# Performance work log

Hardware: AMD Instinct MI355X
Metric: run time of the kernel (lower is better)

## Reference

```python
import jax, jax.numpy as jnp
import numpy as np

N = 100000
E = 1600000
H = 128
L = 3


def setup_inputs() -> dict:
    key = jax.random.key(0)
    ks = jax.random.split(key, 8)
    z = jax.random.normal(ks[0], (N, H), dtype=jnp.float32)
    edge_index = jax.random.randint(ks[1], (2, E), 0, N, dtype=jnp.int64)
    edge_weight = jax.random.uniform(ks[2], (E,), dtype=jnp.float32)
    s = 1.0 / np.sqrt(H)
    weight = jax.random.uniform(ks[3], (L, H, H), minval=-s, maxval=s, dtype=jnp.float32)
    w_ih = jax.random.uniform(ks[4], (3 * H, H), minval=-s, maxval=s, dtype=jnp.float32)
    w_hh = jax.random.uniform(ks[5], (3 * H, H), minval=-s, maxval=s, dtype=jnp.float32)
    b_ih = jax.random.uniform(ks[6], (3 * H,), minval=-s, maxval=s, dtype=jnp.float32)
    b_hh = jax.random.uniform(ks[7], (3 * H,), minval=-s, maxval=s, dtype=jnp.float32)
    return {"z": z, "edge_weight": edge_weight, "weight": weight,
            "w_ih": w_ih, "w_hh": w_hh, "b_ih": b_ih, "b_hh": b_hh,
            "edge_index": edge_index}


def _gru_cell(m, h, w_ih, w_hh, b_ih, b_hh):
    # torch GRUCell: gate order (r, z, n)
    gi = m @ w_ih.T + b_ih   # [N, 3H]
    gh = h @ w_hh.T + b_hh   # [N, 3H]
    i_r, i_z, i_n = jnp.split(gi, 3, axis=-1)
    h_r, h_z, h_n = jnp.split(gh, 3, axis=-1)
    r = jax.nn.sigmoid(i_r + h_r)
    zg = jax.nn.sigmoid(i_z + h_z)
    n = jnp.tanh(i_n + r * h_n)
    return (1.0 - zg) * n + zg * h


def reference(z, edge_weight, weight, w_ih, w_hh, b_ih, b_hh, edge_index):
    src = edge_index[0]  # x_j gathered from source nodes
    dst = edge_index[1]  # aggregated at target nodes
    x = z  # in_channels == out_channels, so no zero padding needed
    for l in range(L):
        m = x @ weight[l]                                  # [N, H]
        msg = m[src] * edge_weight[:, None]                # [E, H]
        agg = jax.ops.segment_sum(msg, dst, num_segments=N)  # aggr='add'
        x = _gru_cell(agg, x, w_ih, w_hh, b_ih, b_hh)
    return x
```

## Files before the change

kernel.cpp:

```cpp
#include <hip/hip_runtime.h>

typedef __bf16 bf16x8 __attribute__((ext_vector_type(8)));
typedef float floatx4 __attribute__((ext_vector_type(4)));

#define NPB 256
#define NPB_SHIFT 8
#define MAXNB 1024
#define TILE 2048

static __device__ __forceinline__ float bfu_to_f(unsigned short u) {
    unsigned int x = ((unsigned int)u) << 16;
    return __builtin_bit_cast(float, x);
}
static __device__ __forceinline__ unsigned short f_to_bfu(float f) {
    unsigned int u = __builtin_bit_cast(unsigned int, f);
    unsigned int r = (u + 0x7fffu + ((u >> 16) & 1u)) >> 16;
    return (unsigned short)r;
}

__global__ void detect_k(const unsigned short* __restrict__ bih_u,
                         const unsigned int* __restrict__ ei_u,
                         int* __restrict__ flags) {
    __shared__ int sv, sz;
    int t = threadIdx.x;
    if (t == 0) { sv = 0; sz = 0; }
    __syncthreads();
    unsigned short u = bih_u[2 * t];
    unsigned int ex = (u >> 7) & 0xFF;
    if (ex >= 64 && ex < 124) atomicAdd(&sv, 1);
    if (ei_u[2 * t + 1] == 0u) atomicAdd(&sz, 1);
    __syncthreads();
    if (t == 0) {
        flags[0] = (sv >= 48) ? 1 : 0;
        flags[1] = (sz == 64) ? 1 : 0;
    }
}


__global__ void cvt_bf16_k(const void* __restrict__ in, unsigned short* __restrict__ out,
                           int n, const int* __restrict__ flags) {
    int i = blockIdx.x * 256 + threadIdx.x;
    if (i >= n) return;
    if (flags[0]) out[i] = ((const unsigned short*)in)[i];
    else out[i] = f_to_bfu(((const float*)in)[i]);
}

__global__ void cvt_bias_k(const void* __restrict__ bih, const void* __restrict__ bhh,
                           float* __restrict__ bih_f, float* __restrict__ bhh_f,
                           const int* __restrict__ flags) {
    int i = blockIdx.x * 256 + threadIdx.x;
    if (i >= 768) return;
    const void* src = (i < 384) ? bih : bhh;
    int j = (i < 384) ? i : i - 384;
    float v = flags[0] ? bfu_to_f(((const unsigned short*)src)[j]) : ((const float*)src)[j];
    if (i < 384) bih_f[j] = v;
    else bhh_f[j] = v;
}

__global__ void out_k(const unsigned short* __restrict__ xb, void* __restrict__ out,
                      int n, const int* __restrict__ flags) {
    int i = blockIdx.x * 256 + threadIdx.x;
    if (i >= n) return;
    if (flags[0]) ((unsigned short*)out)[i] = xb[i];
    else ((float*)out)[i] = bfu_to_f(xb[i]);
}


static __device__ __forceinline__ int load_idx(const unsigned int* eiu, size_t pos, int is64) {
    return (int)eiu[is64 ? 2 * pos : pos];
}

__global__ __launch_bounds__(256) void count_k(const unsigned int* __restrict__ eiu,
                                               int* __restrict__ bucketCnt, int E,
                                               const int* __restrict__ flags) {
    __shared__ int cnt[MAXNB];
    int t = threadIdx.x;
    for (int b = t; b < MAXNB; b += 256) cnt[b] = 0;
    __syncthreads();
    int is64 = flags[1];
    int e0 = blockIdx.x * TILE;
    int e1 = min(e0 + TILE, E);
    for (int e = e0 + t; e < e1; e += 256) {
        int d = load_idx(eiu, (size_t)E + e, is64);
        atomicAdd(&cnt[d >> NPB_SHIFT], 1);
    }
    __syncthreads();
    for (int b = t; b < MAXNB; b += 256) {
        int c = cnt[b];
        if (c) atomicAdd(&bucketCnt[b], c);
    }
}

__global__ void scanB_k(const int* __restrict__ bucketCnt, int* __restrict__ bucketBase,
                        int* __restrict__ bucketCursor, int NB, int E) {
    __shared__ int sh[MAXNB];
    int t = threadIdx.x;
    int v = (t < NB) ? bucketCnt[t] : 0;
    sh[t] = v;
    __syncthreads();
    for (int off = 1; off < MAXNB; off <<= 1) {
        int u = (t >= off) ? sh[t - off] : 0;
        __syncthreads();
        sh[t] += u;
        __syncthreads();
    }
    if (t < NB) {
        int b = sh[t] - v;
        bucketBase[t] = b;
        bucketCursor[t] = b;
    }
    if (t == 0) bucketBase[NB] = E;
}

__global__ __launch_bounds__(256) void bin_k(const unsigned int* __restrict__ eiu,
                                             const void* __restrict__ ew,
                                             int* __restrict__ bucketCursor,
                                             uint2* __restrict__ rec8,
                                             int* __restrict__ dstA, int E,
                                             const int* __restrict__ flags) {
    __shared__ int cnt[MAXNB];
    __shared__ int basel[MAXNB];
    int t = threadIdx.x;
    for (int b = t; b < MAXNB; b += 256) cnt[b] = 0;
    __syncthreads();
    int is64 = flags[1];
    int isb = flags[0];
    int e0 = blockIdx.x * TILE;
    int e1 = min(e0 + TILE, E);
    for (int e = e0 + t; e < e1; e += 256) {
        int d = load_idx(eiu, (size_t)E + e, is64);
        atomicAdd(&cnt[d >> NPB_SHIFT], 1);
    }
    __syncthreads();
    for (int b = t; b < MAXNB; b += 256) {
        int c = cnt[b];
        basel[b] = c ? atomicAdd(&bucketCursor[b], c) : 0;
        cnt[b] = 0;
    }
    __syncthreads();
    for (int e = e0 + t; e < e1; e += 256) {
        int s = load_idx(eiu, (size_t)e, is64);
        int d = load_idx(eiu, (size_t)E + e, is64);
        float w = isb ? bfu_to_f(((const unsigned short*)ew)[e]) : ((const float*)ew)[e];
        int b = d >> NPB_SHIFT;
        int p = basel[b] + atomicAdd(&cnt[b], 1);
        dstA[p] = d;
        rec8[p] = make_uint2((unsigned int)s, __builtin_bit_cast(unsigned int, w));
    }
}

__global__ __launch_bounds__(256) void csr_k(const uint2* __restrict__ rec8,
                                             const int* __restrict__ dstA,
                                             const int* __restrict__ bucketBase,
                                             int* __restrict__ offsets,
                                             uint2* __restrict__ rec, int N, int E) {
    __shared__ int cnt[NPB];
    __shared__ int sh[NPB];
    __shared__ int cur[NPB];
    int t = threadIdx.x;
    int b = blockIdx.x;
    int n0 = b << NPB_SHIFT;
    int nodes = min(NPB, N - n0);
    int ebase = bucketBase[b];
    int ecnt = bucketBase[b + 1] - ebase;

    cnt[t] = 0;
    __syncthreads();
    for (int i = t; i < ecnt; i += 256) {
        int d = dstA[ebase + i] - n0;
        atomicAdd(&cnt[d], 1);
    }
    __syncthreads();
    int v = cnt[t];
    sh[t] = v;
    __syncthreads();
    for (int off = 1; off < NPB; off <<= 1) {
        int u = (t >= off) ? sh[t - off] : 0;
        __syncthreads();
        sh[t] += u;
        __syncthreads();
    }
    int loff = sh[t] - v;
    if (t < nodes) offsets[n0 + t] = ebase + loff;
    cur[t] = ebase + loff;
    if (b == 0 && t == 0) offsets[N] = E;
    __syncthreads();
    for (int i = t; i < ecnt; i += 256) {
        int d = dstA[ebase + i] - n0;
        int p = atomicAdd(&cur[d], 1);
        rec[p] = rec8[ebase + i];
    }
}


static __device__ __forceinline__ float dot8_bf(uint4 wv, uint4 iv) {
    float s;
    s  = bfu_to_f((unsigned short)(wv.x)) * bfu_to_f((unsigned short)(iv.x));
    s += bfu_to_f((unsigned short)(wv.x >> 16)) * bfu_to_f((unsigned short)(iv.x >> 16));
    s += bfu_to_f((unsigned short)(wv.y)) * bfu_to_f((unsigned short)(iv.y));
    s += bfu_to_f((unsigned short)(wv.y >> 16)) * bfu_to_f((unsigned short)(iv.y >> 16));
    s += bfu_to_f((unsigned short)(wv.z)) * bfu_to_f((unsigned short)(iv.z));
    s += bfu_to_f((unsigned short)(wv.z >> 16)) * bfu_to_f((unsigned short)(iv.z >> 16));
    s += bfu_to_f((unsigned short)(wv.w)) * bfu_to_f((unsigned short)(iv.w));
    s += bfu_to_f((unsigned short)(wv.w >> 16)) * bfu_to_f((unsigned short)(iv.w >> 16));
    return s;
}

__global__ void make_ut_k(const void* __restrict__ weight, const void* __restrict__ wih,
                          unsigned short* __restrict__ Ut, const int* __restrict__ flags) {
    int idx = blockIdx.x * 256 + threadIdx.x;
    if (idx >= 3 * 384 * 128) return;
    int isb = flags[0];
    int a = idx & 127;
    int j = (idx >> 7) % 384;
    int l = idx / (384 * 128);
    float s = 0.f;
    if (isb) {
        const uint4* W4 = (const uint4*)((const unsigned short*)weight + (size_t)l * 16384 + a * 128);
        const uint4* I4 = (const uint4*)((const unsigned short*)wih + (size_t)j * 128);
#pragma unroll
        for (int c = 0; c < 16; c++) s += dot8_bf(W4[c], I4[c]);
    } else {
        const float4* W4 = (const float4*)((const float*)weight + (size_t)l * 16384 + a * 128);
        const float4* I4 = (const float4*)((const float*)wih + (size_t)j * 128);
#pragma unroll
        for (int c = 0; c < 32; c++) {
            float4 w = W4[c], i = I4[c];
            s += w.x * i.x + w.y * i.y + w.z * i.z + w.w * i.w;
        }
    }
    Ut[idx] = f_to_bfu(s);
}

__global__ void pack_b_k(const unsigned short* __restrict__ Ut,
                         const void* __restrict__ whh,
                         unsigned short* __restrict__ Bp,
                         const int* __restrict__ flags) {
    int idx = blockIdx.x * 256 + threadIdx.x;
    if (idx >= 3 * 4 * 12 * 4 * 64) return;
    int lane = idx & 63;
    int kc = (idx >> 6) & 3;
    int rest = idx >> 8;
    int j = rest % 12;
    int cg = (rest / 12) & 3;
    int l = rest / 48;
    int s = j / 6;
    int g = (j % 6) >> 1;
    int t = j & 1;
    int col = (cg * 2 + t) * 16 + (lane & 15);
    int k = kc * 32 + (lane >> 4) * 8;
    int row384 = g * 128 + col;
    unsigned short tmp[8];
    const unsigned short* src;
    if (s == 0) {
        src = Ut + (size_t)l * 49152 + row384 * 128 + k;
    } else if (flags[0]) {
        src = (const unsigned short*)whh + (size_t)row384 * 128 + k;
    } else {
        const float* wf = (const float*)whh + (size_t)row384 * 128 + k;
        for (int i = 0; i < 8; i++) tmp[i] = f_to_bfu(wf[i]);
        src = tmp;
    }
    unsigned short* dst = Bp + (size_t)l * 98304 + (((size_t)(cg * 12 + j) * 4 + kc) * 64 + lane) * 8;
    for (int i = 0; i < 8; i++) dst[i] = src[i];
}


__global__ __launch_bounds__(256) void agg_k(const unsigned short* __restrict__ xb,
                                             const int* __restrict__ offs,
                                             const uint2* __restrict__ rec,
                                             unsigned short* __restrict__ y, int N) {
    int node = (int)((blockIdx.x * 256 + threadIdx.x) >> 4);
    int l16 = threadIdx.x & 15;
    if (node >= N) return;
    int b = offs[node];
    int e2 = offs[node + 1];
    const uint4* xp4 = (const uint4*)xb;
    float a0[8], a1[8];
#pragma unroll
    for (int i = 0; i < 8; i++) { a0[i] = 0.f; a1[i] = 0.f; }

    auto fma_row = [&](float* acc, uint4 v, float w) {
        acc[0] += w * __builtin_bit_cast(float, v.x << 16);
        acc[1] += w * __builtin_bit_cast(float, v.x & 0xffff0000u);
        acc[2] += w * __builtin_bit_cast(float, v.y << 16);
        acc[3] += w * __builtin_bit_cast(float, v.y & 0xffff0000u);
        acc[4] += w * __builtin_bit_cast(float, v.z << 16);
        acc[5] += w * __builtin_bit_cast(float, v.z & 0xffff0000u);
        acc[6] += w * __builtin_bit_cast(float, v.w << 16);
        acc[7] += w * __builtin_bit_cast(float, v.w & 0xffff0000u);
    };

    int e = b;
    for (; e + 4 <= e2; e += 4) {
        uint2 r0 = rec[e], r1 = rec[e + 1], r2 = rec[e + 2], r3 = rec[e + 3];
        uint4 v0 = xp4[(size_t)r0.x * 16 + l16];
        uint4 v1 = xp4[(size_t)r1.x * 16 + l16];
        uint4 v2 = xp4[(size_t)r2.x * 16 + l16];
        uint4 v3 = xp4[(size_t)r3.x * 16 + l16];
        fma_row(a0, v0, __builtin_bit_cast(float, r0.y));
        fma_row(a1, v1, __builtin_bit_cast(float, r1.y));
        fma_row(a0, v2, __builtin_bit_cast(float, r2.y));
        fma_row(a1, v3, __builtin_bit_cast(float, r3.y));
    }
    for (; e < e2; e++) {
        uint2 r = rec[e];
        uint4 v = xp4[(size_t)r.x * 16 + l16];
        fma_row(a0, v, __builtin_bit_cast(float, r.y));
    }

    uint4 o;
    o.x = (unsigned int)f_to_bfu(a0[0] + a1[0]) | ((unsigned int)f_to_bfu(a0[1] + a1[1]) << 16);
    o.y = (unsigned int)f_to_bfu(a0[2] + a1[2]) | ((unsigned int)f_to_bfu(a0[3] + a1[3]) << 16);
    o.z = (unsigned int)f_to_bfu(a0[4] + a1[4]) | ((unsigned int)f_to_bfu(a0[5] + a1[5]) << 16);
    o.w = (unsigned int)f_to_bfu(a0[6] + a1[6]) | ((unsigned int)f_to_bfu(a0[7] + a1[7]) << 16);
    ((uint4*)y)[(size_t)node * 16 + l16] = o;
}


__global__ __launch_bounds__(512, 4) void gru_k(const unsigned short* __restrict__ y,
                                                const unsigned short* __restrict__ xin,
                                                unsigned short* __restrict__ xout,
                                                const unsigned short* __restrict__ Bp,
                                                const float* __restrict__ bih,
                                                const float* __restrict__ bhh, int N) {
    __shared__ uint4 Blds[3072];

    int bid = blockIdx.x;
    int r8 = bid & 7;
    int inner = bid >> 3;
    int cg = inner & 3;
    int rb = ((inner >> 2) << 3) + r8;
    int row0 = rb << 7;
    if (row0 >= N) return;

    int tid = threadIdx.x;
    {
        const uint4* bsrc = (const uint4*)(Bp + (size_t)cg * 24576);
#pragma unroll
        for (int i = 0; i < 6; i++) Blds[tid + i * 512] = bsrc[tid + i * 512];
    }
    __syncthreads();

    int wave = tid >> 6;
    int wc = wave & 1;
    int wr = wave >> 1;
    int lane = tid & 63;
    int quad = lane >> 4;
    int m16 = lane & 15;
    const unsigned short* bl = (const unsigned short*)Blds;

    int rA[2];
#pragma unroll
    for (int rt = 0; rt < 2; rt++) {
        int r = row0 + wr * 32 + rt * 16 + m16;
        rA[rt] = (r < N) ? r : N - 1;
    }

    floatx4 acc[2][4];
#pragma unroll
    for (int rt = 0; rt < 2; rt++)
#pragma unroll
        for (int s = 0; s < 4; s++) acc[rt][s] = (floatx4){0.f, 0.f, 0.f, 0.f};

    bf16x8 aY[2][4], aX[2][4];

#pragma unroll
    for (int rt = 0; rt < 2; rt++)
#pragma unroll
        for (int kc = 0; kc < 4; kc++)
            aY[rt][kc] = *(const bf16x8*)(y + (size_t)rA[rt] * 128 + kc * 32 + quad * 8);
    __builtin_amdgcn_sched_barrier(0);

#pragma unroll
    for (int rt = 0; rt < 2; rt++)
#pragma unroll
        for (int kc = 0; kc < 4; kc++)
            aX[rt][kc] = *(const bf16x8*)(xin + (size_t)rA[rt] * 128 + kc * 32 + quad * 8);

#pragma unroll
    for (int kc = 0; kc < 4; kc++) {
#pragma unroll
        for (int g = 0; g < 3; g++) {
            int jU = g * 2 + wc;
            bf16x8 b = *(const bf16x8*)(bl + ((size_t)(jU * 4 + kc) * 64 + lane) * 8);
            int s = (g == 2) ? 2 : g;
            acc[0][s] = __builtin_amdgcn_mfma_f32_16x16x32_bf16(aY[0][kc], b, acc[0][s], 0, 0, 0);
            acc[1][s] = __builtin_amdgcn_mfma_f32_16x16x32_bf16(aY[1][kc], b, acc[1][s], 0, 0, 0);
        }
    }
    __builtin_amdgcn_sched_barrier(0);

#pragma unroll
    for (int kc = 0; kc < 4; kc++) {
#pragma unroll
        for (int g = 0; g < 3; g++) {
            int jW = 6 + g * 2 + wc;
            bf16x8 b = *(const bf16x8*)(bl + ((size_t)(jW * 4 + kc) * 64 + lane) * 8);
            int s = (g == 2) ? 3 : g;
            acc[0][s] = __builtin_amdgcn_mfma_f32_16x16x32_bf16(aX[0][kc], b, acc[0][s], 0, 0, 0);
            acc[1][s] = __builtin_amdgcn_mfma_f32_16x16x32_bf16(aX[1][kc], b, acc[1][s], 0, 0, 0);
        }
    }

    int ch = cg * 32 + wc * 16 + m16;
    float b_r = bih[ch] + bhh[ch];
    float b_z = bih[128 + ch] + bhh[128 + ch];
    float bi_n = bih[256 + ch];
    float bh_n = bhh[256 + ch];
#pragma unroll
    for (int rt = 0; rt < 2; rt++) {
#pragma unroll
        for (int ri = 0; ri < 4; ri++) {
            int row = row0 + wr * 32 + rt * 16 + quad * 4 + ri;
            if (row >= N) continue;
            float sr = acc[rt][0][ri] + b_r;
            float sz = acc[rt][1][ri] + b_z;
            float gn = acc[rt][2][ri] + bi_n;
            float hn = acc[rt][3][ri] + bh_n;
            float r = __builtin_amdgcn_rcpf(1.f + __expf(-sr));
            float zg = __builtin_amdgcn_rcpf(1.f + __expf(-sz));
            float x2 = gn + r * hn;
            float n = 1.f - 2.f * __builtin_amdgcn_rcpf(1.f + __expf(2.f * x2));
            float h = bfu_to_f(xin[(size_t)row * 128 + ch]);
            float o = n + zg * (h - n);
            xout[(size_t)row * 128 + ch] = f_to_bfu(o);
        }
    }
}


extern "C" void kernel_launch(void* const* d_in, const int* in_sizes, int n_in,
                              void* d_out, int out_size, void* d_ws, size_t ws_size,
                              hipStream_t stream) {
    const int N = in_sizes[0] / 128;
    const int E = in_sizes[1];
    const int NB = (N + NPB - 1) >> NPB_SHIFT;

    const void* z = d_in[0];
    const void* ew = d_in[1];
    const void* weight = d_in[2];
    const void* wih = d_in[3];
    const void* whh = d_in[4];
    const void* bih = d_in[5];
    const void* bhh = d_in[6];
    const unsigned int* eiu = (const unsigned int*)d_in[7];

    unsigned short* y = (unsigned short*)d_out;

    size_t off = 0;
    char* base = (char*)d_ws;
    auto carve = [&](size_t bytes) -> void* {
        void* p = base + off;
        off = (off + bytes + 255) & ~(size_t)255;
        return p;
    };
    unsigned short* xb = (unsigned short*)carve((size_t)N * 128 * 2);
    unsigned short* xb2 = (unsigned short*)carve((size_t)N * 128 * 2);
    uint2* rec8 = (uint2*)carve((size_t)E * 8);
    int* dstA = (int*)carve((size_t)E * 4);
    uint2* rec = (uint2*)carve((size_t)E * 8);
    int* offsets = (int*)carve((size_t)(N + 1) * 4);
    int* bucketCnt = (int*)carve(MAXNB * 4);
    int* bucketBase = (int*)carve((MAXNB + 1) * 4);
    int* bucketCursor = (int*)carve(MAXNB * 4);
    unsigned short* Ut = (unsigned short*)carve((size_t)3 * 384 * 128 * 2);
    unsigned short* Bp = (unsigned short*)carve((size_t)3 * 48 * 4 * 64 * 8 * 2);
    float* bih_f = (float*)carve(384 * 4);
    float* bhh_f = (float*)carve(384 * 4);
    int* flags = (int*)carve(256);

    detect_k<<<1, 64, 0, stream>>>((const unsigned short*)bih, eiu, flags);

    cvt_bf16_k<<<(N * 128 + 255) / 256, 256, 0, stream>>>(z, xb, N * 128, flags);
    cvt_bias_k<<<3, 256, 0, stream>>>(bih, bhh, bih_f, bhh_f, flags);

    hipMemsetAsync(bucketCnt, 0, MAXNB * 4, stream);
    int gbin = (E + TILE - 1) / TILE;
    count_k<<<gbin, 256, 0, stream>>>(eiu, bucketCnt, E, flags);
    scanB_k<<<1, MAXNB, 0, stream>>>(bucketCnt, bucketBase, bucketCursor, NB, E);
    bin_k<<<gbin, 256, 0, stream>>>(eiu, ew, bucketCursor, rec8, dstA, E, flags);
    csr_k<<<NB, NPB, 0, stream>>>(rec8, dstA, bucketBase, offsets, rec, N, E);

    make_ut_k<<<(3 * 384 * 128 + 255) / 256, 256, 0, stream>>>(weight, wih, Ut, flags);
    pack_b_k<<<(3 * 4 * 12 * 4 * 64 + 255) / 256, 256, 0, stream>>>(Ut, whh, Bp, flags);

    const int RB = (N + 127) >> 7;
    const int grid_gru = 8 * ((RB + 7) >> 3) * 4;

    const unsigned short* cur = xb;
    unsigned short* nxt = xb2;
    for (int l = 0; l < 3; l++) {
        agg_k<<<(N + 15) / 16, 256, 0, stream>>>(cur, offsets, rec, y, N);
        gru_k<<<grid_gru, 512, 0, stream>>>(y, cur, nxt, Bp + (size_t)l * 98304,
                                            bih_f, bhh_f, N);
        const unsigned short* tmp = cur;
        cur = nxt;
        nxt = (unsigned short*)tmp;
    }

    out_k<<<(N * 128 + 255) / 256, 256, 0, stream>>>(cur, d_out, N * 128, flags);
}
```

Before: 653.1 us.

## Pack local dst into edge records, drop dstA, remap agg blocks across XCDs

Packs the low 8 bits of each edge's destination into the upper bits of the source index inside the binned edge record, so the separate dstA array is no longer written or read during CSR construction. This cuts preprocessing memory traffic. It also doubles the binning tile size and permutes agg_k block IDs so consecutive node chunks land on the same XCD, aiming for better L2 locality on offsets and edge records. The risks are that source indices must fit in 20 bits (true for N=100000), and padding blocks that exit early add a little launch overhead.

```diff
diff --git a/kernel.cpp b/kernel.cpp
--- a/kernel.cpp
+++ b/kernel.cpp
@@ -6,7 +6,7 @@
 #define NPB 256
 #define NPB_SHIFT 8
 #define MAXNB 1024
-#define TILE 2048
+#define TILE 4096
 
 static __device__ __forceinline__ float bfu_to_f(unsigned short u) {
     unsigned int x = ((unsigned int)u) << 16;
@@ -115,8 +115,7 @@
 __global__ __launch_bounds__(256) void bin_k(const unsigned int* __restrict__ eiu,
                                              const void* __restrict__ ew,
                                              int* __restrict__ bucketCursor,
-                                             uint2* __restrict__ rec8,
-                                             int* __restrict__ dstA, int E,
+                                             uint2* __restrict__ rec8, int E,
                                              const int* __restrict__ flags) {
     __shared__ int cnt[MAXNB];
     __shared__ int basel[MAXNB];
@@ -144,13 +143,12 @@
         float w = isb ? bfu_to_f(((const unsigned short*)ew)[e]) : ((const float*)ew)[e];
         int b = d >> NPB_SHIFT;
         int p = basel[b] + atomicAdd(&cnt[b], 1);
-        dstA[p] = d;
-        rec8[p] = make_uint2((unsigned int)s, __builtin_bit_cast(unsigned int, w));
+        rec8[p] = make_uint2((unsigned int)s | ((unsigned int)(d & 255) << 20),
+                             __builtin_bit_cast(unsigned int, w));
     }
 }
 
 __global__ __launch_bounds__(256) void csr_k(const uint2* __restrict__ rec8,
-                                             const int* __restrict__ dstA,
                                              const int* __restrict__ bucketBase,
                                              int* __restrict__ offsets,
                                              uint2* __restrict__ rec, int N, int E) {
@@ -167,7 +165,7 @@
     cnt[t] = 0;
     __syncthreads();
     for (int i = t; i < ecnt; i += 256) {
-        int d = dstA[ebase + i] - n0;
+        int d = (rec8[ebase + i].x >> 20) & 255;
         atomicAdd(&cnt[d], 1);
     }
     __syncthreads();
@@ -186,9 +184,10 @@
     if (b == 0 && t == 0) offsets[N] = E;
     __syncthreads();
     for (int i = t; i < ecnt; i += 256) {
-        int d = dstA[ebase + i] - n0;
+        uint2 r = rec8[ebase + i];
+        int d = (r.x >> 20) & 255;
         int p = atomicAdd(&cur[d], 1);
-        rec[p] = rec8[ebase + i];
+        rec[p] = make_uint2(r.x & 0xFFFFFu, r.y);
     }
 }
 
@@ -269,8 +268,12 @@
 __global__ __launch_bounds__(256) void agg_k(const unsigned short* __restrict__ xb,
                                              const int* __restrict__ offs,
                                              const uint2* __restrict__ rec,
-                                             unsigned short* __restrict__ y, int N) {
-    int node = (int)((blockIdx.x * 256 + threadIdx.x) >> 4);
+                                             unsigned short* __restrict__ y, int N,
+                                             int nch) {
+    int bid = blockIdx.x;
+    int c = ((bid & 7) << 3) + ((bid >> 3) & 7) + ((bid >> 6) << 6);
+    if (c >= nch) return;
+    int node = c * 16 + (threadIdx.x >> 4);
     int l16 = threadIdx.x & 15;
     if (node >= N) return;
     int b = offs[node];
@@ -458,7 +461,6 @@
     unsigned short* xb = (unsigned short*)carve((size_t)N * 128 * 2);
     unsigned short* xb2 = (unsigned short*)carve((size_t)N * 128 * 2);
     uint2* rec8 = (uint2*)carve((size_t)E * 8);
-    int* dstA = (int*)carve((size_t)E * 4);
     uint2* rec = (uint2*)carve((size_t)E * 8);
     int* offsets = (int*)carve((size_t)(N + 1) * 4);
     int* bucketCnt = (int*)carve(MAXNB * 4);
@@ -479,19 +481,21 @@
     int gbin = (E + TILE - 1) / TILE;
     count_k<<<gbin, 256, 0, stream>>>(eiu, bucketCnt, E, flags);
     scanB_k<<<1, MAXNB, 0, stream>>>(bucketCnt, bucketBase, bucketCursor, NB, E);
-    bin_k<<<gbin, 256, 0, stream>>>(eiu, ew, bucketCursor, rec8, dstA, E, flags);
-    csr_k<<<NB, NPB, 0, stream>>>(rec8, dstA, bucketBase, offsets, rec, N, E);
+    bin_k<<<gbin, 256, 0, stream>>>(eiu, ew, bucketCursor, rec8, E, flags);
+    csr_k<<<NB, NPB, 0, stream>>>(rec8, bucketBase, offsets, rec, N, E);
 
     make_ut_k<<<(3 * 384 * 128 + 255) / 256, 256, 0, stream>>>(weight, wih, Ut, flags);
     pack_b_k<<<(3 * 4 * 12 * 4 * 64 + 255) / 256, 256, 0, stream>>>(Ut, whh, Bp, flags);
 
     const int RB = (N + 127) >> 7;
     const int grid_gru = 8 * ((RB + 7) >> 3) * 4;
+    const int nch = (N + 15) >> 4;
+    const int grid_agg = ((nch + 63) >> 6) << 6;
 
     const unsigned short* cur = xb;
     unsigned short* nxt = xb2;
     for (int l = 0; l < 3; l++) {
-        agg_k<<<(N + 15) / 16, 256, 0, stream>>>(cur, offsets, rec, y, N);
+        agg_k<<<grid_agg, 256, 0, stream>>>(cur, offsets, rec, y, N, nch);
         gru_k<<<grid_gru, 512, 0, stream>>>(y, cur, nxt, Bp + (size_t)l * 98304,
                                             bih_f, bhh_f, N);
         const unsigned short* tmp = cur;
```

Result: faster. 607.4 us (-7.0%).
